# Kernel optimization log

Hardware: AMD Instinct MI355X
Metric: run time of the kernel (lower is better)

Reference implementation:

```python
import jax, jax.numpy as jnp
import numpy as np

H, IN, L, R = 128, 64, 3, 7
Nc, Na, Nx = 10000, 40000, 100000
NS = (Nc, Na, Nx)
ES = (50000, 100000, 100000, 150000, 200000, 200000, 200000)
# relation order: cc, c->a, a->c, aa, a->x, x->a, xx  (0=core,1=agg,2=access)
SRC_T = (0, 0, 1, 1, 1, 2, 2)
DST_T = (0, 1, 0, 1, 2, 1, 2)


def setup_inputs() -> dict:
    key = jax.random.key(0)
    ks = iter(jax.random.split(key, 80))
    d = {}
    for name, n in (("x_core", Nc), ("x_agg", Na), ("x_access", Nx)):
        d[name] = jax.random.normal(next(ks), (n, IN), jnp.float32)
    for r in range(R):
        d[f"src{r}"] = jax.random.randint(next(ks), (ES[r],), 0, NS[SRC_T[r]])
        d[f"dst{r}"] = jax.random.randint(next(ks), (ES[r],), 0, NS[DST_T[r]])
        d[f"ea{r}"] = jax.random.normal(next(ks), (ES[r], 3), jnp.float32)

    def w(k, shape, fan):
        return (jax.random.normal(k, shape, jnp.float32) / np.float32(np.sqrt(fan)))

    for nt in ("core", "agg", "access"):
        d[f"linW_{nt}"] = w(next(ks), (IN, H), IN)
        d[f"linb_{nt}"] = jnp.zeros((H,), jnp.float32)
    d["eW"] = w(next(ks), (L, R, 3, H), 3)       # GINEConv edge Linear(3->H)
    d["eb"] = jnp.zeros((L, R, H), jnp.float32)
    d["W1"] = w(next(ks), (L, R, H, H), H)        # MLP first Linear
    d["b1"] = jnp.zeros((L, R, H), jnp.float32)
    d["g1"] = jnp.ones((L, R, H), jnp.float32)    # BatchNorm gamma
    d["be1"] = jnp.zeros((L, R, H), jnp.float32)  # BatchNorm beta
    d["W2"] = w(next(ks), (L, R, H, H), H)        # MLP second Linear
    d["b2"] = jnp.zeros((L, R, H), jnp.float32)
    return d


def _forward(x_core, x_agg, x_access,
             linW_core, linb_core, linW_agg, linb_agg, linW_access, linb_access,
             eW, eb, W1, b1, g1, be1, W2, b2, srcs, dsts, eas):
    elu = jax.nn.elu
    h = [elu(x_core @ linW_core + linb_core),
         elu(x_agg @ linW_agg + linb_agg),
         elu(x_access @ linW_access + linb_access)]
    bn_inv = 1.0 / jnp.sqrt(jnp.float32(1.0 + 1e-5))  # eval BN: running mean 0, var 1
    for l in range(L):
        out = [jnp.zeros_like(ht) for ht in h]
        for r in range(R):
            s, t = SRC_T[r], DST_T[r]
            # GINEConv message: ReLU(x_j + Lin(edge_attr))  -> [E, H]
            msg = jax.nn.relu(h[s][srcs[r]] + eas[r] @ eW[l, r] + eb[l, r])
            agg = jax.ops.segment_sum(msg, dsts[r], num_segments=h[t].shape[0])
            z = h[t] + agg  # (1+eps)*x_i + aggr, eps=0
            # PyG MLP([H,H,H]): Linear -> BatchNorm -> ReLU -> Linear
            z = jax.nn.relu((z @ W1[l, r] + b1[l, r]) * bn_inv * g1[l, r] + be1[l, r])
            out[t] = out[t] + (z @ W2[l, r] + b2[l, r])  # HeteroConv aggr='sum'
        # residual + ELU; dropout is identity in eval mode
        h = [elu(out[t] + h[t]) for t in range(3)]
    return tuple(h)


def reference(x_core, x_agg, x_access,
              src0, dst0, ea0, src1, dst1, ea1, src2, dst2, ea2,
              src3, dst3, ea3, src4, dst4, ea4, src5, dst5, ea5,
              src6, dst6, ea6,
              linW_core, linb_core, linW_agg, linb_agg, linW_access, linb_access,
              eW, eb, W1, b1, g1, be1, W2, b2):
    srcs = (src0, src1, src2, src3, src4, src5, src6)
    dsts = (dst0, dst1, dst2, dst3, dst4, dst5, dst6)
    eas = (ea0, ea1, ea2, ea3, ea4, ea5, ea6)
    return _forward(x_core, x_agg, x_access,
                    linW_core, linb_core, linW_agg, linb_agg, linW_access, linb_access,
                    eW, eb, W1, b1, g1, be1, W2, b2, srcs, dsts, eas)
```

## Files before the change

### kernel.cpp

```cpp
#include <hip/hip_runtime.h>
#include <math.h>

#define H 128

typedef __attribute__((ext_vector_type(8))) short short8;
typedef __attribute__((ext_vector_type(4))) float f32x4;

static const int SRC_T_[7] = {0, 0, 1, 1, 1, 2, 2};
static const int DST_T_[7] = {0, 1, 0, 1, 2, 1, 2};

__device__ __forceinline__ float eluf(float x) {
    return x > 0.f ? x : (__expf(x) - 1.f);
}
__device__ __forceinline__ unsigned short f2bf(float x) {
    union { float f; unsigned int u; } v; v.f = x;
    unsigned int r = v.u + 0x7fffu + ((v.u >> 16) & 1u);
    return (unsigned short)(r >> 16);
}
__device__ __forceinline__ float bf2f(unsigned int u) {
    union { unsigned int u; float f; } v; v.u = u << 16;
    return v.f;
}

#define GLDS16(gp, lp) __builtin_amdgcn_global_load_lds( \
    (const __attribute__((address_space(1))) void*)(gp), \
    (__attribute__((address_space(3))) void*)(lp), 16, 0, 0)

__global__ __launch_bounds__(128) void k_input_linear(
    const float* __restrict__ x, const float* __restrict__ W,
    const float* __restrict__ b, unsigned short* __restrict__ hb, int n)
{
    __shared__ float Ws[64 * H];
    __shared__ float xs[16 * 64];
    __shared__ unsigned short os[16 * H];
    const int j = threadIdx.x;
    for (int i = j; i < 64 * H; i += 128) Ws[i] = W[i];
    const float bj = b[j];

    for (int r0 = blockIdx.x * 16; r0 < n; r0 += gridDim.x * 16) {
        const int nrows = min(16, n - r0);
        __syncthreads();
        for (int i = j; i < nrows * 64; i += 128) xs[i] = x[(size_t)r0 * 64 + i];
        __syncthreads();
        for (int i = 0; i < nrows; ++i) {
            float acc = bj;
#pragma unroll
            for (int k = 0; k < 64; k += 4) {
                float4 xv = *(const float4*)&xs[i * 64 + k];
                acc += xv.x * Ws[(k + 0) * H + j] + xv.y * Ws[(k + 1) * H + j]
                     + xv.z * Ws[(k + 2) * H + j] + xv.w * Ws[(k + 3) * H + j];
            }
            os[i * H + j] = f2bf(eluf(acc));
        }
        __syncthreads();
        uint2* d = (uint2*)&hb[(size_t)r0 * H];
        const uint2* s2 = (const uint2*)os;
        for (int i = j; i < nrows * 32; i += 128) d[i] = s2[i];
    }
}

struct CsrCtx {
    const int* src[7]; const int* dst[7]; const float* ea[7];
    int* csr_src[7]; uint2* csr_ea[7]; int* ptr[7];
    int* deg; int* cursor; int* bsum;
    int eOff[8];
    int bOff[8];
    int nd[7];
};

__global__ __launch_bounds__(256) void k_hist_all(CsrCtx C, int Etot)
{
    for (int e = blockIdx.x * 256 + threadIdx.x; e < Etot; e += gridDim.x * 256) {
        int r = 0;
        while (e >= C.eOff[r + 1]) ++r;
        const int le = e - C.eOff[r];
        atomicAdd(&C.deg[(C.bOff[r] << 8) + C.dst[r][le]], 1);
    }
}

__global__ __launch_bounds__(256) void k_scan_partial_all(CsrCtx C)
{
    __shared__ int s[256];
    const int b = blockIdx.x;
    int r = 0;
    while (b >= C.bOff[r + 1]) ++r;
    const int lb = b - C.bOff[r];
    const int tid = threadIdx.x;
    const int idx = lb * 256 + tid;
    s[tid] = idx < C.nd[r] ? C.deg[(C.bOff[r] << 8) + idx] : 0;
    __syncthreads();
    for (int off = 128; off > 0; off >>= 1) {
        if (tid < off) s[tid] += s[tid + off];
        __syncthreads();
    }
    if (tid == 0) C.bsum[b] = s[0];
}

__global__ __launch_bounds__(512) void k_scan_mid_all(CsrCtx C)
{
    __shared__ int s[512];
    const int r = blockIdx.x;
    const int nb = C.bOff[r + 1] - C.bOff[r];
    const int tid = threadIdx.x;
    const int v = tid < nb ? C.bsum[C.bOff[r] + tid] : 0;
    s[tid] = v;
    __syncthreads();
    for (int off = 1; off < 512; off <<= 1) {
        int t = (tid >= off) ? s[tid - off] : 0;
        __syncthreads();
        s[tid] += t;
        __syncthreads();
    }
    if (tid < nb) C.bsum[C.bOff[r] + tid] = s[tid] - v;
    if (tid == nb - 1) C.ptr[r][C.nd[r]] = s[tid];
}

__global__ __launch_bounds__(256) void k_scan_final_all(CsrCtx C)
{
    __shared__ int s[256];
    const int b = blockIdx.x;
    int r = 0;
    while (b >= C.bOff[r + 1]) ++r;
    const int lb = b - C.bOff[r];
    const int tid = threadIdx.x;
    const int idx = lb * 256 + tid;
    const int v = idx < C.nd[r] ? C.deg[(C.bOff[r] << 8) + idx] : 0;
    s[tid] = v;
    __syncthreads();
    for (int off = 1; off < 256; off <<= 1) {
        int t = (tid >= off) ? s[tid - off] : 0;
        __syncthreads();
        s[tid] += t;
        __syncthreads();
    }
    if (idx < C.nd[r]) {
        const int excl = s[tid] - v + C.bsum[b];
        C.ptr[r][idx] = excl;
        C.cursor[(C.bOff[r] << 8) + idx] = excl;
    }
}

__global__ __launch_bounds__(256) void k_scatter_all(CsrCtx C, int Etot)
{
    for (int e = blockIdx.x * 256 + threadIdx.x; e < Etot; e += gridDim.x * 256) {
        int r = 0;
        while (e >= C.eOff[r + 1]) ++r;
        const int le = e - C.eOff[r];
        const int d = C.dst[r][le];
        const int pos = atomicAdd(&C.cursor[(C.bOff[r] << 8) + d], 1);
        C.csr_src[r][pos] = C.src[r][le];
        const float* eap = C.ea[r] + (size_t)3 * le;
        uint2 p;
        p.x = (unsigned int)f2bf(eap[0]) | ((unsigned int)f2bf(eap[1]) << 16);
        p.y = (unsigned int)f2bf(eap[2]);
        C.csr_ea[r][pos] = p;
    }
}

__global__ __launch_bounds__(256) void k_wprep(
    const float* __restrict__ W1, const float* __restrict__ W2,
    unsigned short* __restrict__ wp, int total)
{
    for (int i = blockIdx.x * 256 + threadIdx.x; i < total; i += gridDim.x * 256) {
        int lr = i >> 14, rem = i & 16383;
        int c = rem >> 7, k = rem & 127;
        wp[(size_t)(lr * 2 + 0) * 16384 + rem] = f2bf(W1[(size_t)lr * 16384 + k * H + c]);
        wp[(size_t)(lr * 2 + 1) * 16384 + rem] = f2bf(W2[(size_t)lr * 16384 + k * H + c]);
    }
}

struct AggCtx {
    const int* ptr[7]; const int* csr_src[7]; const uint2* csr_ea[7];
    const unsigned short* hsrc[7]; const unsigned short* hdst[7];
    unsigned short* z[7];
    int gOff[8];
    int nd[7];
};

__global__ __launch_bounds__(256) void k_aggz_all(
    AggCtx A, const float* __restrict__ eW, const float* __restrict__ eb, int l)
{
    const int b = blockIdx.x;
    int r = 0;
    while (b >= A.gOff[r + 1]) ++r;
    const int lb = b - A.gOff[r];
    const int wave = threadIdx.x >> 6;
    const int lane = threadIdx.x & 63;
    const int t2 = lane << 1;
    const int lr = l * 7 + r;
    const float* eWr = eW + (size_t)lr * 3 * H;
    const float* ebr = eb + (size_t)lr * H;
    const float w00 = eWr[t2],         w01 = eWr[t2 + 1];
    const float w10 = eWr[H + t2],     w11 = eWr[H + t2 + 1];
    const float w20 = eWr[2 * H + t2], w21 = eWr[2 * H + t2 + 1];
    const float b0 = ebr[t2], b1v = ebr[t2 + 1];

    const int nd = A.nd[r];
    const int d0 = lb * 64 + wave * 16;
    if (d0 >= nd) return;
    const int dend = min(d0 + 16, nd);
    const int* __restrict__ ptr = A.ptr[r];
    const int* __restrict__ cs = A.csr_src[r];
    const uint2* __restrict__ ce = A.csr_ea[r];
    const unsigned short* __restrict__ hs = A.hsrc[r];
    const unsigned short* __restrict__ hd = A.hdst[r];
    unsigned int* __restrict__ zp = (unsigned int*)A.z[r];

    int p1 = ptr[d0];
    for (int d = d0; d < dend; ++d) {
        const int p0 = p1;
        p1 = ptr[d + 1];
        const unsigned int hdv = ((const unsigned int*)&hd[(size_t)d * H])[lane];
        float acc0 = bf2f(hdv & 0xffffu);
        float acc1 = bf2f(hdv >> 16);
        int i = p0;
        for (; i + 1 < p1; i += 2) {
            const int s0 = cs[i], s1 = cs[i + 1];
            const uint2 e0 = ce[i], e1 = ce[i + 1];
            const unsigned int hv0 = ((const unsigned int*)&hs[(size_t)s0 * H])[lane];
            const unsigned int hv1 = ((const unsigned int*)&hs[(size_t)s1 * H])[lane];
            const float a00 = bf2f(e0.x & 0xffffu), a01 = bf2f(e0.x >> 16), a02 = bf2f(e0.y & 0xffffu);
            const float a10 = bf2f(e1.x & 0xffffu), a11 = bf2f(e1.x >> 16), a12 = bf2f(e1.y & 0xffffu);
            acc0 += fmaxf(bf2f(hv0 & 0xffffu) + a00 * w00 + a01 * w10 + a02 * w20 + b0, 0.f)
                  + fmaxf(bf2f(hv1 & 0xffffu) + a10 * w00 + a11 * w10 + a12 * w20 + b0, 0.f);
            acc1 += fmaxf(bf2f(hv0 >> 16) + a00 * w01 + a01 * w11 + a02 * w21 + b1v, 0.f)
                  + fmaxf(bf2f(hv1 >> 16) + a10 * w01 + a11 * w11 + a12 * w21 + b1v, 0.f);
        }
        if (i < p1) {
            const int s = cs[i];
            const uint2 ep = ce[i];
            const float a0 = bf2f(ep.x & 0xffffu);
            const float a1 = bf2f(ep.x >> 16);
            const float a2 = bf2f(ep.y & 0xffffu);
            const unsigned int hv = ((const unsigned int*)&hs[(size_t)s * H])[lane];
            acc0 += fmaxf(bf2f(hv & 0xffffu) + a0 * w00 + a1 * w10 + a2 * w20 + b0, 0.f);
            acc1 += fmaxf(bf2f(hv >> 16)     + a0 * w01 + a1 * w11 + a2 * w21 + b1v, 0.f);
        }
        zp[(size_t)d * 64 + (lane ^ ((d & 7) << 2))] =
            (unsigned int)f2bf(acc0) | ((unsigned int)f2bf(acc1) << 16);
    }
}

struct MlpCtx {
    const unsigned short* z[3][3];
    int lr[3][3];
    int nrel[3];
    int gend[3];
    int noffH[3];
    int n[3];
};

__global__ __launch_bounds__(512, 4) void k_mlp_all(
    MlpCtx M, const unsigned short* __restrict__ hb,
    unsigned short* __restrict__ hbw, float* __restrict__ fout,
    const unsigned short* __restrict__ wprep,
    const float* __restrict__ b1g, const float* __restrict__ g1g,
    const float* __restrict__ be1g, const float* __restrict__ b2g, int fin)
{
    __shared__ unsigned short zt[128 * H];
    __shared__ unsigned short a1t[128 * H];

    const int b = blockIdx.x;
    const int t = (b >= M.gend[0] ? 1 : 0) + (b >= M.gend[1] ? 1 : 0);
    const int lb = b - (t == 0 ? 0 : M.gend[t - 1]);
    const int n = M.n[t];
    const int nrel = M.nrel[t];
    const unsigned short* hbp = hb + (size_t)M.noffH[t];

    const int tid = threadIdx.x;
    const int lane = tid & 63;
    const int wave = tid >> 6;
    const int wr = wave >> 2;
    const int wc = wave & 3;
    const int l15 = lane & 15;
    const int lq  = lane >> 4;
    const int c0 = wc * 32 + l15;

    const int r0 = lb * 128;
    const int rows = min(128, n - r0);
    const bool full = (rows == 128);

    auto stage = [&](const unsigned short* z) {
        const unsigned short* zsrc = z + (size_t)r0 * H;
        if (full) {
#pragma unroll
            for (int it = 0; it < 4; ++it) {
                const int off = (wave * 4 + it) * 512;
                GLDS16(zsrc + off + lane * 8, zt + off);
            }
        } else {
            for (int idx = tid; idx < rows * 16; idx += 512) {
                *(uint4*)&zt[idx * 8] = *(const uint4*)&zsrc[idx * 8];
            }
        }
    };

    const float bn_inv = 0.99999500003749977f;
    const f32x4 Z4 = {0.f, 0.f, 0.f, 0.f};
    f32x4 acc2[4][2];
#pragma unroll
    for (int rb = 0; rb < 4; ++rb)
#pragma unroll
        for (int nf = 0; nf < 2; ++nf) acc2[rb][nf] = Z4;
    float b2s0 = 0.f, b2s1 = 0.f;

    stage(M.z[t][0]);

    for (int rl = 0; rl < nrel; ++rl) {
        const int lr = M.lr[t][rl];
        const unsigned short* wp = wprep + (size_t)lr * 32768;
        short8 w1f[2][4];
#pragma unroll
        for (int nf = 0; nf < 2; ++nf)
#pragma unroll
            for (int kc = 0; kc < 4; ++kc)
                w1f[nf][kc] = *(const short8*)&wp[(c0 + nf * 16) * H + kc * 32 + (lq << 3)];
        const float b1c0 = b1g[lr * H + c0],            b1c1 = b1g[lr * H + c0 + 16];
        const float sc0  = g1g[lr * H + c0] * bn_inv,   sc1  = g1g[lr * H + c0 + 16] * bn_inv;
        const float be0  = be1g[lr * H + c0],           be1v = be1g[lr * H + c0 + 16];
        b2s0 += b2g[lr * H + c0]; b2s1 += b2g[lr * H + c0 + 16];

        __syncthreads();

        f32x4 acc1[4][2];
#pragma unroll
        for (int rb = 0; rb < 4; ++rb)
#pragma unroll
            for (int nf = 0; nf < 2; ++nf) acc1[rb][nf] = Z4;
#pragma unroll
        for (int kc = 0; kc < 4; ++kc) {
            const int kb = kc * 32 + (lq << 3);
            short8 af[4];
#pragma unroll
            for (int rb = 0; rb < 4; ++rb) {
                const int row = wr * 64 + rb * 16 + l15;
                af[rb] = *(const short8*)&zt[row * H + (kb ^ ((row & 7) << 3))];
            }
#pragma unroll
            for (int rb = 0; rb < 4; ++rb)
#pragma unroll
                for (int nf = 0; nf < 2; ++nf)
                    acc1[rb][nf] = __builtin_amdgcn_mfma_f32_16x16x32_bf16(
                        af[rb], w1f[nf][kc], acc1[rb][nf], 0, 0, 0);
        }
#pragma unroll
        for (int rb = 0; rb < 4; ++rb)
#pragma unroll
            for (int nf = 0; nf < 2; ++nf) {
                const int col = c0 + nf * 16;
                const float b1c = nf == 0 ? b1c0 : b1c1;
                const float scv = nf == 0 ? sc0 : sc1;
                const float bev = nf == 0 ? be0 : be1v;
#pragma unroll
                for (int rg = 0; rg < 4; ++rg) {
                    const int row = wr * 64 + rb * 16 + (lq << 2) + rg;
                    float v = fmaxf((acc1[rb][nf][rg] + b1c) * scv + bev, 0.f);
                    a1t[row * H + (col ^ ((row & 7) << 3))] = f2bf(v);
                }
            }
        __syncthreads();

        if (rl + 1 < nrel) stage(M.z[t][rl + 1]);

#pragma unroll
        for (int kc = 0; kc < 4; ++kc) {
            const int kb = kc * 32 + (lq << 3);
            short8 af[4], wf[2];
#pragma unroll
            for (int rb = 0; rb < 4; ++rb) {
                const int row = wr * 64 + rb * 16 + l15;
                af[rb] = *(const short8*)&a1t[row * H + (kb ^ ((row & 7) << 3))];
            }
#pragma unroll
            for (int nf = 0; nf < 2; ++nf)
                wf[nf] = *(const short8*)&wp[16384 + (c0 + nf * 16) * H + kb];
#pragma unroll
            for (int rb = 0; rb < 4; ++rb)
#pragma unroll
                for (int nf = 0; nf < 2; ++nf)
                    acc2[rb][nf] = __builtin_amdgcn_mfma_f32_16x16x32_bf16(
                        af[rb], wf[nf], acc2[rb][nf], 0, 0, 0);
        }
    }

    if (fin) {
        float* foutp = fout + (size_t)M.noffH[t];
#pragma unroll
        for (int rb = 0; rb < 4; ++rb)
#pragma unroll
            for (int nf = 0; nf < 2; ++nf) {
                const int col = c0 + nf * 16;
                const float b2s = nf == 0 ? b2s0 : b2s1;
#pragma unroll
                for (int rg = 0; rg < 4; ++rg) {
                    const int row = wr * 64 + rb * 16 + (lq << 2) + rg;
                    if (row < rows) {
                        const size_t o = (size_t)(r0 + row) * H + col;
                        foutp[o] = eluf(acc2[rb][nf][rg] + b2s
                                        + bf2f((unsigned int)hbp[o]));
                    }
                }
            }
    } else {
        unsigned short* hbwp = hbw + (size_t)M.noffH[t];
        __syncthreads();
#pragma unroll
        for (int rb = 0; rb < 4; ++rb)
#pragma unroll
            for (int nf = 0; nf < 2; ++nf) {
                const int col = c0 + nf * 16;
                const float b2s = nf == 0 ? b2s0 : b2s1;
#pragma unroll
                for (int rg = 0; rg < 4; ++rg) {
                    const int row = wr * 64 + rb * 16 + (lq << 2) + rg;
                    if (row < rows) {
                        const size_t o = (size_t)(r0 + row) * H + col;
                        a1t[row * H + col] = f2bf(eluf(acc2[rb][nf][rg] + b2s
                                                       + bf2f((unsigned int)hbp[o])));
                    }
                }
            }
        __syncthreads();
        uint2* d = (uint2*)&hbwp[(size_t)r0 * H];
        const uint2* s2 = (const uint2*)a1t;
        for (int idx = tid; idx < rows * 32; idx += 512) d[idx] = s2[idx];
    }
}

static inline int imin(int a, int b) { return a < b ? a : b; }
static inline size_t alignup(size_t x) { return (x + 255) & ~(size_t)255; }

extern "C" void kernel_launch(void* const* d_in, const int* in_sizes, int n_in,
                              void* d_out, int out_size, void* d_ws, size_t ws_size,
                              hipStream_t stream) {
    const float* xin[3] = {(const float*)d_in[0], (const float*)d_in[1], (const float*)d_in[2]};
    const int* src[7]; const int* dst[7]; const float* ea[7]; int E[7];
    for (int r = 0; r < 7; ++r) {
        src[r] = (const int*)d_in[3 + 3 * r];
        dst[r] = (const int*)d_in[4 + 3 * r];
        ea[r]  = (const float*)d_in[5 + 3 * r];
        E[r]   = in_sizes[3 + 3 * r];
    }
    const float* linW[3] = {(const float*)d_in[24], (const float*)d_in[26], (const float*)d_in[28]};
    const float* linb[3] = {(const float*)d_in[25], (const float*)d_in[27], (const float*)d_in[29]};
    const float* eW  = (const float*)d_in[30];
    const float* ebp = (const float*)d_in[31];
    const float* W1  = (const float*)d_in[32];
    const float* b1  = (const float*)d_in[33];
    const float* g1  = (const float*)d_in[34];
    const float* be1 = (const float*)d_in[35];
    const float* W2  = (const float*)d_in[36];
    const float* b2  = (const float*)d_in[37];

    const int NSn[3]  = {in_sizes[0] / 64, in_sizes[1] / 64, in_sizes[2] / 64};
    const int NTOT = NSn[0] + NSn[1] + NSn[2];
    const int noff[3] = {0, NSn[0], NSn[0] + NSn[1]};

    float* fout = (float*)d_out;

    int eOff[8]; eOff[0] = 0;
    for (int r = 0; r < 7; ++r) eOff[r + 1] = eOff[r] + E[r];
    const int Etot = eOff[7];
    int bOff[8]; bOff[0] = 0;
    for (int r = 0; r < 7; ++r) bOff[r + 1] = bOff[r] + (NSn[DST_T_[r]] + 255) / 256;
    int gOff[8]; gOff[0] = 0;
    for (int r = 0; r < 7; ++r) gOff[r + 1] = gOff[r] + (NSn[DST_T_[r]] + 63) / 64;

    char* wsb = (char*)d_ws;
    size_t off = 0;
    unsigned short* hb = (unsigned short*)(wsb + off); off = alignup(off + (size_t)NTOT * H * 2);
    unsigned short* zb[7];
    for (int r = 0; r < 7; ++r) {
        int nd = NSn[DST_T_[r]];
        zb[r] = (unsigned short*)(wsb + off); off = alignup(off + (size_t)nd * H * 2);
    }
    unsigned short* wprep = (unsigned short*)(wsb + off); off = alignup(off + (size_t)21 * 32768 * 2);
    int* deg    = (int*)(wsb + off); off = alignup(off + (size_t)bOff[7] * 256 * 4);
    int* cursor = (int*)(wsb + off); off = alignup(off + (size_t)bOff[7] * 256 * 4);
    int* bsum   = (int*)(wsb + off); off = alignup(off + (size_t)bOff[7] * 4 + 256);
    int* ptrs[7]; int* csrs[7]; uint2* ceas[7];
    for (int r = 0; r < 7; ++r) {
        int nd = NSn[DST_T_[r]];
        ptrs[r] = (int*)(wsb + off); off = alignup(off + (size_t)(nd + 1) * 4);
    }
    for (int r = 0; r < 7; ++r) {
        csrs[r] = (int*)(wsb + off); off = alignup(off + (size_t)E[r] * 4);
    }
    for (int r = 0; r < 7; ++r) {
        ceas[r] = (uint2*)(wsb + off); off = alignup(off + (size_t)E[r] * 8);
    }

    CsrCtx C;
    for (int r = 0; r < 7; ++r) {
        C.src[r] = src[r]; C.dst[r] = dst[r]; C.ea[r] = ea[r];
        C.csr_src[r] = csrs[r]; C.csr_ea[r] = ceas[r]; C.ptr[r] = ptrs[r];
        C.nd[r] = NSn[DST_T_[r]];
    }
    C.deg = deg; C.cursor = cursor; C.bsum = bsum;
    for (int r = 0; r < 8; ++r) { C.eOff[r] = eOff[r]; C.bOff[r] = bOff[r]; }

    hipMemsetAsync(deg, 0, (size_t)bOff[7] * 256 * 4, stream);
    k_hist_all<<<imin((Etot + 255) / 256, 8192), 256, 0, stream>>>(C, Etot);
    k_scan_partial_all<<<bOff[7], 256, 0, stream>>>(C);
    k_scan_mid_all<<<7, 512, 0, stream>>>(C);
    k_scan_final_all<<<bOff[7], 256, 0, stream>>>(C);
    k_scatter_all<<<imin((Etot + 255) / 256, 8192), 256, 0, stream>>>(C, Etot);
    k_wprep<<<1344, 256, 0, stream>>>(W1, W2, wprep, 21 * 16384);

    for (int t = 0; t < 3; ++t) {
        int n = NSn[t];
        k_input_linear<<<imin((n + 15) / 16, 2048), 128, 0, stream>>>(
            xin[t], linW[t], linb[t], hb + (size_t)noff[t] * H, n);
    }

    AggCtx A;
    for (int r = 0; r < 7; ++r) {
        A.ptr[r] = ptrs[r]; A.csr_src[r] = csrs[r]; A.csr_ea[r] = ceas[r];
        A.hsrc[r] = hb + (size_t)noff[SRC_T_[r]] * H;
        A.hdst[r] = hb + (size_t)noff[DST_T_[r]] * H;
        A.z[r] = zb[r];
        A.nd[r] = NSn[DST_T_[r]];
    }
    for (int r = 0; r < 8; ++r) A.gOff[r] = gOff[r];

    static const int RELS[3][3] = {{0, 2, 0}, {1, 3, 5}, {4, 6, 0}};
    static const int NRELS[3] = {2, 3, 2};
    MlpCtx M;
    int gend = 0;
    for (int t = 0; t < 3; ++t) {
        M.nrel[t] = NRELS[t];
        M.noffH[t] = noff[t] * H;
        M.n[t] = NSn[t];
        gend += (NSn[t] + 127) / 128;
        M.gend[t] = gend;
        for (int k = 0; k < 3; ++k) M.z[t][k] = zb[RELS[t][k]];
    }

    for (int l = 0; l < 3; ++l) {
        const int fin = (l == 2) ? 1 : 0;
        k_aggz_all<<<gOff[7], 256, 0, stream>>>(A, eW, ebp, l);
        for (int t = 0; t < 3; ++t)
            for (int k = 0; k < 3; ++k) M.lr[t][k] = l * 7 + RELS[t][k];
        k_mlp_all<<<M.gend[2], 512, 0, stream>>>(
            M, hb, hb, fout, wprep, b1, g1, be1, b2, fin);
    }
}
```

Measured before the change: 896.3 us.

## Fuse edge aggregation into per-layer MLP kernel with ping-pong hidden buffers

Removes the separate aggregation kernel and the per-relation z buffers. Each MLP block now gathers neighbour messages for its own 128 destination rows straight into shared memory before the matmuls, and zero-fills the tail rows. This avoids a global write and re-read of every z tile and one launch per layer. Hidden states now alternate between two buffers, so a block cannot overwrite rows that other blocks are still gathering. The cost is that the latency-bound gather now runs in LDS-heavy 512-thread blocks at lower occupancy, and it no longer overlaps the asynchronous z prefetch.

```diff
diff --git a/kernel.cpp b/kernel.cpp
--- a/kernel.cpp
+++ b/kernel.cpp
@@ -21,10 +21,6 @@
     union { unsigned int u; float f; } v; v.u = u << 16;
     return v.f;
 }
-
-#define GLDS16(gp, lp) __builtin_amdgcn_global_load_lds( \
-    (const __attribute__((address_space(1))) void*)(gp), \
-    (__attribute__((address_space(3))) void*)(lp), 16, 0, 0)
 
 __global__ __launch_bounds__(128) void k_input_linear(
     const float* __restrict__ x, const float* __restrict__ W,
@@ -169,103 +165,36 @@
     }
 }
 
-struct AggCtx {
-    const int* ptr[7]; const int* csr_src[7]; const uint2* csr_ea[7];
-    const unsigned short* hsrc[7]; const unsigned short* hdst[7];
-    unsigned short* z[7];
-    int gOff[8];
-    int nd[7];
-};
-
-__global__ __launch_bounds__(256) void k_aggz_all(
-    AggCtx A, const float* __restrict__ eW, const float* __restrict__ eb, int l)
-{
-    const int b = blockIdx.x;
-    int r = 0;
-    while (b >= A.gOff[r + 1]) ++r;
-    const int lb = b - A.gOff[r];
-    const int wave = threadIdx.x >> 6;
-    const int lane = threadIdx.x & 63;
-    const int t2 = lane << 1;
-    const int lr = l * 7 + r;
-    const float* eWr = eW + (size_t)lr * 3 * H;
-    const float* ebr = eb + (size_t)lr * H;
-    const float w00 = eWr[t2],         w01 = eWr[t2 + 1];
-    const float w10 = eWr[H + t2],     w11 = eWr[H + t2 + 1];
-    const float w20 = eWr[2 * H + t2], w21 = eWr[2 * H + t2 + 1];
-    const float b0 = ebr[t2], b1v = ebr[t2 + 1];
-
-    const int nd = A.nd[r];
-    const int d0 = lb * 64 + wave * 16;
-    if (d0 >= nd) return;
-    const int dend = min(d0 + 16, nd);
-    const int* __restrict__ ptr = A.ptr[r];
-    const int* __restrict__ cs = A.csr_src[r];
-    const uint2* __restrict__ ce = A.csr_ea[r];
-    const unsigned short* __restrict__ hs = A.hsrc[r];
-    const unsigned short* __restrict__ hd = A.hdst[r];
-    unsigned int* __restrict__ zp = (unsigned int*)A.z[r];
-
-    int p1 = ptr[d0];
-    for (int d = d0; d < dend; ++d) {
-        const int p0 = p1;
-        p1 = ptr[d + 1];
-        const unsigned int hdv = ((const unsigned int*)&hd[(size_t)d * H])[lane];
-        float acc0 = bf2f(hdv & 0xffffu);
-        float acc1 = bf2f(hdv >> 16);
-        int i = p0;
-        for (; i + 1 < p1; i += 2) {
-            const int s0 = cs[i], s1 = cs[i + 1];
-            const uint2 e0 = ce[i], e1 = ce[i + 1];
-            const unsigned int hv0 = ((const unsigned int*)&hs[(size_t)s0 * H])[lane];
-            const unsigned int hv1 = ((const unsigned int*)&hs[(size_t)s1 * H])[lane];
-            const float a00 = bf2f(e0.x & 0xffffu), a01 = bf2f(e0.x >> 16), a02 = bf2f(e0.y & 0xffffu);
-            const float a10 = bf2f(e1.x & 0xffffu), a11 = bf2f(e1.x >> 16), a12 = bf2f(e1.y & 0xffffu);
-            acc0 += fmaxf(bf2f(hv0 & 0xffffu) + a00 * w00 + a01 * w10 + a02 * w20 + b0, 0.f)
-                  + fmaxf(bf2f(hv1 & 0xffffu) + a10 * w00 + a11 * w10 + a12 * w20 + b0, 0.f);
-            acc1 += fmaxf(bf2f(hv0 >> 16) + a00 * w01 + a01 * w11 + a02 * w21 + b1v, 0.f)
-                  + fmaxf(bf2f(hv1 >> 16) + a10 * w01 + a11 * w11 + a12 * w21 + b1v, 0.f);
-        }
-        if (i < p1) {
-            const int s = cs[i];
-            const uint2 ep = ce[i];
-            const float a0 = bf2f(ep.x & 0xffffu);
-            const float a1 = bf2f(ep.x >> 16);
-            const float a2 = bf2f(ep.y & 0xffffu);
-            const unsigned int hv = ((const unsigned int*)&hs[(size_t)s * H])[lane];
-            acc0 += fmaxf(bf2f(hv & 0xffffu) + a0 * w00 + a1 * w10 + a2 * w20 + b0, 0.f);
-            acc1 += fmaxf(bf2f(hv >> 16)     + a0 * w01 + a1 * w11 + a2 * w21 + b1v, 0.f);
-        }
-        zp[(size_t)d * 64 + (lane ^ ((d & 7) << 2))] =
-            (unsigned int)f2bf(acc0) | ((unsigned int)f2bf(acc1) << 16);
-    }
-}
-
-struct MlpCtx {
-    const unsigned short* z[3][3];
-    int lr[3][3];
+struct LayerCtx {
+    const int* ptr[3][3];
+    const int* csr_src[3][3];
+    const uint2* csr_ea[3][3];
+    int srcOffH[3][3];
+    int rel[3][3];
     int nrel[3];
     int gend[3];
     int noffH[3];
     int n[3];
 };
 
-__global__ __launch_bounds__(512, 4) void k_mlp_all(
-    MlpCtx M, const unsigned short* __restrict__ hb,
-    unsigned short* __restrict__ hbw, float* __restrict__ fout,
+__global__ __launch_bounds__(512, 4) void k_layer_all(
+    LayerCtx L, const unsigned short* __restrict__ hin,
+    unsigned short* __restrict__ hout, float* __restrict__ fout,
     const unsigned short* __restrict__ wprep,
+    const float* __restrict__ eWg, const float* __restrict__ ebg,
     const float* __restrict__ b1g, const float* __restrict__ g1g,
-    const float* __restrict__ be1g, const float* __restrict__ b2g, int fin)
+    const float* __restrict__ be1g, const float* __restrict__ b2g,
+    int l, int fin)
 {
     __shared__ unsigned short zt[128 * H];
     __shared__ unsigned short a1t[128 * H];
 
     const int b = blockIdx.x;
-    const int t = (b >= M.gend[0] ? 1 : 0) + (b >= M.gend[1] ? 1 : 0);
-    const int lb = b - (t == 0 ? 0 : M.gend[t - 1]);
-    const int n = M.n[t];
-    const int nrel = M.nrel[t];
-    const unsigned short* hbp = hb + (size_t)M.noffH[t];
+    const int t = (b >= L.gend[0] ? 1 : 0) + (b >= L.gend[1] ? 1 : 0);
+    const int lb = b - (t == 0 ? 0 : L.gend[t - 1]);
+    const int n = L.n[t];
+    const int nrel = L.nrel[t];
+    const unsigned short* hinp = hin + (size_t)L.noffH[t];
 
     const int tid = threadIdx.x;
     const int lane = tid & 63;
@@ -275,25 +204,10 @@
     const int l15 = lane & 15;
     const int lq  = lane >> 4;
     const int c0 = wc * 32 + l15;
+    const int t2 = lane << 1;
 
     const int r0 = lb * 128;
     const int rows = min(128, n - r0);
-    const bool full = (rows == 128);
-
-    auto stage = [&](const unsigned short* z) {
-        const unsigned short* zsrc = z + (size_t)r0 * H;
-        if (full) {
-#pragma unroll
-            for (int it = 0; it < 4; ++it) {
-                const int off = (wave * 4 + it) * 512;
-                GLDS16(zsrc + off + lane * 8, zt + off);
-            }
-        } else {
-            for (int idx = tid; idx < rows * 16; idx += 512) {
-                *(uint4*)&zt[idx * 8] = *(const uint4*)&zsrc[idx * 8];
-            }
-        }
-    };
 
     const float bn_inv = 0.99999500003749977f;
     const f32x4 Z4 = {0.f, 0.f, 0.f, 0.f};
@@ -304,11 +218,62 @@
         for (int nf = 0; nf < 2; ++nf) acc2[rb][nf] = Z4;
     float b2s0 = 0.f, b2s1 = 0.f;
 
-    stage(M.z[t][0]);
-
     for (int rl = 0; rl < nrel; ++rl) {
-        const int lr = M.lr[t][rl];
+        const int lr = l * 7 + L.rel[t][rl];
         const unsigned short* wp = wprep + (size_t)lr * 32768;
+
+        {
+            const int* __restrict__ ptr = L.ptr[t][rl];
+            const int* __restrict__ cs = L.csr_src[t][rl];
+            const uint2* __restrict__ ce = L.csr_ea[t][rl];
+            const unsigned short* __restrict__ hs = hin + (size_t)L.srcOffH[t][rl];
+            const float* eWr = eWg + (size_t)lr * 3 * H;
+            const float* ebr = ebg + (size_t)lr * H;
+            const float w00 = eWr[t2],         w01 = eWr[t2 + 1];
+            const float w10 = eWr[H + t2],     w11 = eWr[H + t2 + 1];
+            const float w20 = eWr[2 * H + t2], w21 = eWr[2 * H + t2 + 1];
+            const float b0 = ebr[t2], b1e = ebr[t2 + 1];
+            unsigned int* __restrict__ ztu = (unsigned int*)zt;
+
+            const int d0 = r0 + wave * 16;
+            const int dend = min(d0 + 16, n);
+            int p1v = (d0 < dend) ? ptr[d0] : 0;
+            for (int d = d0; d < dend; ++d) {
+                const int p0 = p1v;
+                p1v = ptr[d + 1];
+                const unsigned int hdv = ((const unsigned int*)&hinp[(size_t)d * H])[lane];
+                float acc0 = bf2f(hdv & 0xffffu);
+                float acc1 = bf2f(hdv >> 16);
+                int i = p0;
+                for (; i + 1 < p1v; i += 2) {
+                    const int s0 = cs[i], s1 = cs[i + 1];
+                    const uint2 e0 = ce[i], e1 = ce[i + 1];
+                    const unsigned int hv0 = ((const unsigned int*)&hs[(size_t)s0 * H])[lane];
+                    const unsigned int hv1 = ((const unsigned int*)&hs[(size_t)s1 * H])[lane];
+                    const float a00 = bf2f(e0.x & 0xffffu), a01 = bf2f(e0.x >> 16), a02 = bf2f(e0.y & 0xffffu);
+                    const float a10 = bf2f(e1.x & 0xffffu), a11 = bf2f(e1.x >> 16), a12 = bf2f(e1.y & 0xffffu);
+                    acc0 += fmaxf(bf2f(hv0 & 0xffffu) + a00 * w00 + a01 * w10 + a02 * w20 + b0, 0.f)
+                          + fmaxf(bf2f(hv1 & 0xffffu) + a10 * w00 + a11 * w10 + a12 * w20 + b0, 0.f);
+                    acc1 += fmaxf(bf2f(hv0 >> 16) + a00 * w01 + a01 * w11 + a02 * w21 + b1e, 0.f)
+                          + fmaxf(bf2f(hv1 >> 16) + a10 * w01 + a11 * w11 + a12 * w21 + b1e, 0.f);
+                }
+                if (i < p1v) {
+                    const int s = cs[i];
+                    const uint2 ep = ce[i];
+                    const float a0 = bf2f(ep.x & 0xffffu);
+                    const float a1 = bf2f(ep.x >> 16);
+                    const float a2 = bf2f(ep.y & 0xffffu);
+                    const unsigned int hv = ((const unsigned int*)&hs[(size_t)s * H])[lane];
+                    acc0 += fmaxf(bf2f(hv & 0xffffu) + a0 * w00 + a1 * w10 + a2 * w20 + b0, 0.f);
+                    acc1 += fmaxf(bf2f(hv >> 16)     + a0 * w01 + a1 * w11 + a2 * w21 + b1e, 0.f);
+                }
+                ztu[(size_t)(d - r0) * 64 + (lane ^ ((d & 7) << 2))] =
+                    (unsigned int)f2bf(acc0) | ((unsigned int)f2bf(acc1) << 16);
+            }
+            for (int d = (dend > d0 ? dend : d0); d < d0 + 16; ++d)
+                ztu[(size_t)(d - r0) * 64 + lane] = 0;
+        }
+
         short8 w1f[2][4];
 #pragma unroll
         for (int nf = 0; nf < 2; ++nf)
@@ -360,8 +325,6 @@
             }
         __syncthreads();
 
-        if (rl + 1 < nrel) stage(M.z[t][rl + 1]);
-
 #pragma unroll
         for (int kc = 0; kc < 4; ++kc) {
             const int kb = kc * 32 + (lq << 3);
@@ -384,7 +347,7 @@
     }
 
     if (fin) {
-        float* foutp = fout + (size_t)M.noffH[t];
+        float* foutp = fout + (size_t)L.noffH[t];
 #pragma unroll
         for (int rb = 0; rb < 4; ++rb)
 #pragma unroll
@@ -397,12 +360,12 @@
                     if (row < rows) {
                         const size_t o = (size_t)(r0 + row) * H + col;
                         foutp[o] = eluf(acc2[rb][nf][rg] + b2s
-                                        + bf2f((unsigned int)hbp[o]));
+                                        + bf2f((unsigned int)hinp[o]));
                     }
                 }
             }
     } else {
-        unsigned short* hbwp = hbw + (size_t)M.noffH[t];
+        unsigned short* houtp = hout + (size_t)L.noffH[t];
         __syncthreads();
 #pragma unroll
         for (int rb = 0; rb < 4; ++rb)
@@ -416,12 +379,12 @@
                     if (row < rows) {
                         const size_t o = (size_t)(r0 + row) * H + col;
                         a1t[row * H + col] = f2bf(eluf(acc2[rb][nf][rg] + b2s
-                                                       + bf2f((unsigned int)hbp[o])));
+                                                       + bf2f((unsigned int)hinp[o])));
                     }
                 }
             }
         __syncthreads();
-        uint2* d = (uint2*)&hbwp[(size_t)r0 * H];
+        uint2* d = (uint2*)&houtp[(size_t)r0 * H];
         const uint2* s2 = (const uint2*)a1t;
         for (int idx = tid; idx < rows * 32; idx += 512) d[idx] = s2[idx];
     }
@@ -463,17 +426,11 @@
     const int Etot = eOff[7];
     int bOff[8]; bOff[0] = 0;
     for (int r = 0; r < 7; ++r) bOff[r + 1] = bOff[r] + (NSn[DST_T_[r]] + 255) / 256;
-    int gOff[8]; gOff[0] = 0;
-    for (int r = 0; r < 7; ++r) gOff[r + 1] = gOff[r] + (NSn[DST_T_[r]] + 63) / 64;
 
     char* wsb = (char*)d_ws;
     size_t off = 0;
-    unsigned short* hb = (unsigned short*)(wsb + off); off = alignup(off + (size_t)NTOT * H * 2);
-    unsigned short* zb[7];
-    for (int r = 0; r < 7; ++r) {
-        int nd = NSn[DST_T_[r]];
-        zb[r] = (unsigned short*)(wsb + off); off = alignup(off + (size_t)nd * H * 2);
-    }
+    unsigned short* hb0 = (unsigned short*)(wsb + off); off = alignup(off + (size_t)NTOT * H * 2);
+    unsigned short* hb1 = (unsigned short*)(wsb + off); off = alignup(off + (size_t)NTOT * H * 2);
     unsigned short* wprep = (unsigned short*)(wsb + off); off = alignup(off + (size_t)21 * 32768 * 2);
     int* deg    = (int*)(wsb + off); off = alignup(off + (size_t)bOff[7] * 256 * 4);
     int* cursor = (int*)(wsb + off); off = alignup(off + (size_t)bOff[7] * 256 * 4);
@@ -510,38 +467,35 @@
     for (int t = 0; t < 3; ++t) {
         int n = NSn[t];
         k_input_linear<<<imin((n + 15) / 16, 2048), 128, 0, stream>>>(
-            xin[t], linW[t], linb[t], hb + (size_t)noff[t] * H, n);
-    }
-
-    AggCtx A;
-    for (int r = 0; r < 7; ++r) {
-        A.ptr[r] = ptrs[r]; A.csr_src[r] = csrs[r]; A.csr_ea[r] = ceas[r];
-        A.hsrc[r] = hb + (size_t)noff[SRC_T_[r]] * H;
-        A.hdst[r] = hb + (size_t)noff[DST_T_[r]] * H;
-        A.z[r] = zb[r];
-        A.nd[r] = NSn[DST_T_[r]];
-    }
-    for (int r = 0; r < 8; ++r) A.gOff[r] = gOff[r];
+            xin[t], linW[t], linb[t], hb0 + (size_t)noff[t] * H, n);
+    }
 
     static const int RELS[3][3] = {{0, 2, 0}, {1, 3, 5}, {4, 6, 0}};
     static const int NRELS[3] = {2, 3, 2};
-    MlpCtx M;
+    LayerCtx L;
     int gend = 0;
     for (int t = 0; t < 3; ++t) {
-        M.nrel[t] = NRELS[t];
-        M.noffH[t] = noff[t] * H;
-        M.n[t] = NSn[t];
+        L.nrel[t] = NRELS[t];
+        L.noffH[t] = noff[t] * H;
+        L.n[t] = NSn[t];
         gend += (NSn[t] + 127) / 128;
-        M.gend[t] = gend;
-        for (int k = 0; k < 3; ++k) M.z[t][k] = zb[RELS[t][k]];
-    }
-
+        L.gend[t] = gend;
+        for (int k = 0; k < 3; ++k) {
+            const int r = RELS[t][k];
+            L.ptr[t][k] = ptrs[r];
+            L.csr_src[t][k] = csrs[r];
+            L.csr_ea[t][k] = ceas[r];
+            L.srcOffH[t][k] = noff[SRC_T_[r]] * H;
+            L.rel[t][k] = r;
+        }
+    }
+
+    unsigned short* hin = hb0;
+    unsigned short* hout = hb1;
     for (int l = 0; l < 3; ++l) {
         const int fin = (l == 2) ? 1 : 0;
-        k_aggz_all<<<gOff[7], 256, 0, stream>>>(A, eW, ebp, l);
-        for (int t = 0; t < 3; ++t)
-            for (int k = 0; k < 3; ++k) M.lr[t][k] = l * 7 + RELS[t][k];
-        k_mlp_all<<<M.gend[2], 512, 0, stream>>>(
-            M, hb, hb, fout, wprep, b1, g1, be1, b2, fin);
-    }
-}
+        k_layer_all<<<L.gend[2], 512, 0, stream>>>(
+            L, hin, hout, fout, wprep, eW, ebp, b1, g1, be1, b2, l, fin);
+        unsigned short* tmp = hin; hin = hout; hout = tmp;
+    }
+}
```

After: 1.185 ms. 32.2% more time.

## Merge histogram, input linear and weight prep into one launch; prefetch edges in aggregation

Applied to the files above, without the earlier changes.

Folds the degree histogram, the three per-type input linear kernels and the weight bf16 transposition into a single kernel that splits its blocks by role. This removes several launches and lets these independent jobs run at the same time. The input linear now uses one 256-thread block per 16 rows, with no grid-stride loop, and each half of the block computes 8 rows. Separately, the aggregation loop software-pipelines its gathers by loading the next pair of edges before computing the current pair, to hide gather latency at the cost of extra registers.

```diff
diff --git a/kernel.cpp b/kernel.cpp
--- a/kernel.cpp
+++ b/kernel.cpp
@@ -26,23 +26,48 @@
     (const __attribute__((address_space(1))) void*)(gp), \
     (__attribute__((address_space(3))) void*)(lp), 16, 0, 0)
 
-__global__ __launch_bounds__(128) void k_input_linear(
-    const float* __restrict__ x, const float* __restrict__ W,
-    const float* __restrict__ b, unsigned short* __restrict__ hb, int n)
+struct PreCtx {
+    const int* dst[7];
+    int* deg;
+    int eOff[8], bOff[8];
+    const float* x[3]; const float* linW[3]; const float* linb[3];
+    unsigned short* hb[3]; int n[3];
+    const float* W1; const float* W2; unsigned short* wp;
+    int gHist, gIn[3], gEnd;
+};
+
+__global__ __launch_bounds__(256) void k_pre(PreCtx P, int Etot)
 {
     __shared__ float Ws[64 * H];
     __shared__ float xs[16 * 64];
     __shared__ unsigned short os[16 * H];
-    const int j = threadIdx.x;
-    for (int i = j; i < 64 * H; i += 128) Ws[i] = W[i];
-    const float bj = b[j];
-
-    for (int r0 = blockIdx.x * 16; r0 < n; r0 += gridDim.x * 16) {
+    const int b = blockIdx.x;
+    const int tid = threadIdx.x;
+
+    if (b < P.gHist) {
+        for (int e = b * 256 + tid; e < Etot; e += P.gHist * 256) {
+            int r = 0;
+            while (e >= P.eOff[r + 1]) ++r;
+            atomicAdd(&P.deg[(P.bOff[r] << 8) + P.dst[r][e - P.eOff[r]]], 1);
+        }
+        return;
+    }
+    if (b < P.gIn[2]) {
+        const int t = (b >= P.gIn[0] ? 1 : 0) + (b >= P.gIn[1] ? 1 : 0);
+        const int lb = b - (t == 0 ? P.gHist : P.gIn[t - 1]);
+        const float* x = P.x[t];
+        const float* W = P.linW[t];
+        const int n = P.n[t];
+        const int j = tid & 127;
+        const int half = tid >> 7;
+        for (int i = tid; i < 64 * H; i += 256) Ws[i] = W[i];
+        const float bj = P.linb[t][j];
+        const int r0 = lb * 16;
         const int nrows = min(16, n - r0);
-        __syncthreads();
-        for (int i = j; i < nrows * 64; i += 128) xs[i] = x[(size_t)r0 * 64 + i];
-        __syncthreads();
-        for (int i = 0; i < nrows; ++i) {
+        for (int i = tid; i < nrows * 64; i += 256) xs[i] = x[(size_t)r0 * 64 + i];
+        __syncthreads();
+        for (int i = half * 8; i < half * 8 + 8; ++i) {
+            if (i >= nrows) break;
             float acc = bj;
 #pragma unroll
             for (int k = 0; k < 64; k += 4) {
@@ -53,9 +78,20 @@
             os[i * H + j] = f2bf(eluf(acc));
         }
         __syncthreads();
-        uint2* d = (uint2*)&hb[(size_t)r0 * H];
+        uint2* d = (uint2*)&P.hb[t][(size_t)r0 * H];
         const uint2* s2 = (const uint2*)os;
-        for (int i = j; i < nrows * 32; i += 128) d[i] = s2[i];
+        for (int i = tid; i < nrows * 32; i += 256) d[i] = s2[i];
+        return;
+    }
+    {
+        const int lb = b - P.gIn[2];
+        const int gw = P.gEnd - P.gIn[2];
+        for (int i = lb * 256 + tid; i < 21 * 16384; i += gw * 256) {
+            int lr = i >> 14, rem = i & 16383;
+            int c = rem >> 7, k = rem & 127;
+            P.wp[(size_t)(lr * 2 + 0) * 16384 + rem] = f2bf(P.W1[(size_t)lr * 16384 + k * H + c]);
+            P.wp[(size_t)(lr * 2 + 1) * 16384 + rem] = f2bf(P.W2[(size_t)lr * 16384 + k * H + c]);
+        }
     }
 }
 
@@ -67,16 +103,6 @@
     int bOff[8];
     int nd[7];
 };
-
-__global__ __launch_bounds__(256) void k_hist_all(CsrCtx C, int Etot)
-{
-    for (int e = blockIdx.x * 256 + threadIdx.x; e < Etot; e += gridDim.x * 256) {
-        int r = 0;
-        while (e >= C.eOff[r + 1]) ++r;
-        const int le = e - C.eOff[r];
-        atomicAdd(&C.deg[(C.bOff[r] << 8) + C.dst[r][le]], 1);
-    }
-}
 
 __global__ __launch_bounds__(256) void k_scan_partial_all(CsrCtx C)
 {
@@ -154,18 +180,6 @@
         p.x = (unsigned int)f2bf(eap[0]) | ((unsigned int)f2bf(eap[1]) << 16);
         p.y = (unsigned int)f2bf(eap[2]);
         C.csr_ea[r][pos] = p;
-    }
-}
-
-__global__ __launch_bounds__(256) void k_wprep(
-    const float* __restrict__ W1, const float* __restrict__ W2,
-    unsigned short* __restrict__ wp, int total)
-{
-    for (int i = blockIdx.x * 256 + threadIdx.x; i < total; i += gridDim.x * 256) {
-        int lr = i >> 14, rem = i & 16383;
-        int c = rem >> 7, k = rem & 127;
-        wp[(size_t)(lr * 2 + 0) * 16384 + rem] = f2bf(W1[(size_t)lr * 16384 + k * H + c]);
-        wp[(size_t)(lr * 2 + 1) * 16384 + rem] = f2bf(W2[(size_t)lr * 16384 + k * H + c]);
     }
 }
 
@@ -208,23 +222,37 @@
 
     int p1 = ptr[d0];
     for (int d = d0; d < dend; ++d) {
-        const int p0 = p1;
+        const int p0v = p1;
         p1 = ptr[d + 1];
         const unsigned int hdv = ((const unsigned int*)&hd[(size_t)d * H])[lane];
         float acc0 = bf2f(hdv & 0xffffu);
         float acc1 = bf2f(hdv >> 16);
-        int i = p0;
-        for (; i + 1 < p1; i += 2) {
-            const int s0 = cs[i], s1 = cs[i + 1];
-            const uint2 e0 = ce[i], e1 = ce[i + 1];
-            const unsigned int hv0 = ((const unsigned int*)&hs[(size_t)s0 * H])[lane];
-            const unsigned int hv1 = ((const unsigned int*)&hs[(size_t)s1 * H])[lane];
-            const float a00 = bf2f(e0.x & 0xffffu), a01 = bf2f(e0.x >> 16), a02 = bf2f(e0.y & 0xffffu);
-            const float a10 = bf2f(e1.x & 0xffffu), a11 = bf2f(e1.x >> 16), a12 = bf2f(e1.y & 0xffffu);
-            acc0 += fmaxf(bf2f(hv0 & 0xffffu) + a00 * w00 + a01 * w10 + a02 * w20 + b0, 0.f)
-                  + fmaxf(bf2f(hv1 & 0xffffu) + a10 * w00 + a11 * w10 + a12 * w20 + b0, 0.f);
-            acc1 += fmaxf(bf2f(hv0 >> 16) + a00 * w01 + a01 * w11 + a02 * w21 + b1v, 0.f)
-                  + fmaxf(bf2f(hv1 >> 16) + a10 * w01 + a11 * w11 + a12 * w21 + b1v, 0.f);
+        int i = p0v;
+        if (i + 1 < p1) {
+            int s0 = cs[i], s1 = cs[i + 1];
+            uint2 eC0 = ce[i], eC1 = ce[i + 1];
+            unsigned int hvC0 = ((const unsigned int*)&hs[(size_t)s0 * H])[lane];
+            unsigned int hvC1 = ((const unsigned int*)&hs[(size_t)s1 * H])[lane];
+            for (;;) {
+                const int jn = i + 2;
+                const bool more = (jn + 1 < p1);
+                uint2 eN0, eN1; unsigned int hvN0 = 0, hvN1 = 0;
+                if (more) {
+                    const int sN0 = cs[jn], sN1 = cs[jn + 1];
+                    eN0 = ce[jn]; eN1 = ce[jn + 1];
+                    hvN0 = ((const unsigned int*)&hs[(size_t)sN0 * H])[lane];
+                    hvN1 = ((const unsigned int*)&hs[(size_t)sN1 * H])[lane];
+                }
+                const float a00 = bf2f(eC0.x & 0xffffu), a01 = bf2f(eC0.x >> 16), a02 = bf2f(eC0.y & 0xffffu);
+                const float a10 = bf2f(eC1.x & 0xffffu), a11 = bf2f(eC1.x >> 16), a12 = bf2f(eC1.y & 0xffffu);
+                acc0 += fmaxf(bf2f(hvC0 & 0xffffu) + a00 * w00 + a01 * w10 + a02 * w20 + b0, 0.f)
+                      + fmaxf(bf2f(hvC1 & 0xffffu) + a10 * w00 + a11 * w10 + a12 * w20 + b0, 0.f);
+                acc1 += fmaxf(bf2f(hvC0 >> 16) + a00 * w01 + a01 * w11 + a02 * w21 + b1v, 0.f)
+                      + fmaxf(bf2f(hvC1 >> 16) + a10 * w01 + a11 * w11 + a12 * w21 + b1v, 0.f);
+                i = jn;
+                if (!more) break;
+                eC0 = eN0; eC1 = eN1; hvC0 = hvN0; hvC1 = hvN1;
+            }
         }
         if (i < p1) {
             const int s = cs[i];
@@ -490,6 +518,23 @@
         ceas[r] = (uint2*)(wsb + off); off = alignup(off + (size_t)E[r] * 8);
     }
 
+    PreCtx P;
+    for (int r = 0; r < 7; ++r) P.dst[r] = dst[r];
+    P.deg = deg;
+    for (int r = 0; r < 8; ++r) { P.eOff[r] = eOff[r]; P.bOff[r] = bOff[r]; }
+    for (int t = 0; t < 3; ++t) {
+        P.x[t] = xin[t]; P.linW[t] = linW[t]; P.linb[t] = linb[t];
+        P.hb[t] = hb + (size_t)noff[t] * H; P.n[t] = NSn[t];
+    }
+    P.W1 = W1; P.W2 = W2; P.wp = wprep;
+    P.gHist = 1024;
+    int g = P.gHist;
+    for (int t = 0; t < 3; ++t) { g += (NSn[t] + 15) / 16; P.gIn[t] = g; }
+    P.gEnd = g + 336;
+
+    hipMemsetAsync(deg, 0, (size_t)bOff[7] * 256 * 4, stream);
+    k_pre<<<P.gEnd, 256, 0, stream>>>(P, Etot);
+
     CsrCtx C;
     for (int r = 0; r < 7; ++r) {
         C.src[r] = src[r]; C.dst[r] = dst[r]; C.ea[r] = ea[r];
@@ -499,19 +544,10 @@
     C.deg = deg; C.cursor = cursor; C.bsum = bsum;
     for (int r = 0; r < 8; ++r) { C.eOff[r] = eOff[r]; C.bOff[r] = bOff[r]; }
 
-    hipMemsetAsync(deg, 0, (size_t)bOff[7] * 256 * 4, stream);
-    k_hist_all<<<imin((Etot + 255) / 256, 8192), 256, 0, stream>>>(C, Etot);
     k_scan_partial_all<<<bOff[7], 256, 0, stream>>>(C);
     k_scan_mid_all<<<7, 512, 0, stream>>>(C);
     k_scan_final_all<<<bOff[7], 256, 0, stream>>>(C);
     k_scatter_all<<<imin((Etot + 255) / 256, 8192), 256, 0, stream>>>(C, Etot);
-    k_wprep<<<1344, 256, 0, stream>>>(W1, W2, wprep, 21 * 16384);
-
-    for (int t = 0; t < 3; ++t) {
-        int n = NSn[t];
-        k_input_linear<<<imin((n + 15) / 16, 2048), 128, 0, stream>>>(
-            xin[t], linW[t], linb[t], hb + (size_t)noff[t] * H, n);
-    }
 
     AggCtx A;
     for (int r = 0; r < 7; ++r) {
```

Result: faster. 843.0 us (-6.0%).
